# Performance work log

Hardware: AMD Instinct MI355X
Metric: run time of the kernel (lower is better)

## Reference

```python
import jax, jax.numpy as jnp
import numpy as np

B, T, D = 4, 4096, 1024


def setup_inputs() -> dict:
    key = jax.random.key(0)
    ks = jax.random.split(key, 7)
    s_in = 1.0 / np.sqrt(D)
    return {
        "x": jax.random.normal(ks[0], (B, T, D), dtype=jnp.float32),
        "W_in": jax.random.uniform(ks[1], (D, 2 * D), jnp.float32, -s_in, s_in),
        "b_in": jax.random.uniform(ks[2], (2 * D,), jnp.float32, -s_in, s_in),
        "A": jax.random.normal(ks[3], (D,), dtype=jnp.float32),
        "C": jax.random.normal(ks[4], (D,), dtype=jnp.float32),
        "W_out": jax.random.uniform(ks[5], (D, D), jnp.float32, -s_in, s_in),
        "b_out": jax.random.uniform(ks[6], (D,), jnp.float32, -s_in, s_in),
    }


def _ssm(v, A, C):
    # diagonal linear recurrence: h_t = sigmoid(A) * h_{t-1} + v_t ; y_t = C * h_t
    decay = jax.nn.sigmoid(A)  # (D,)
    vT = jnp.swapaxes(v, 0, 1)  # (T, B, D)

    def step(h, vt):
        h = decay * h + vt
        return h, h

    h0 = jnp.zeros(vT.shape[1:], dtype=v.dtype)
    _, hs = jax.lax.scan(step, h0, vT)  # (T, B, D)
    return jnp.swapaxes(hs, 0, 1) * C  # (B, T, D)


def reference(x, W_in, b_in, A, C, W_out, b_out):
    proj = x @ W_in + b_in  # (B, T, 2D)
    v, gate = jnp.split(proj, 2, axis=-1)
    gate = jax.nn.sigmoid(gate)
    y = gate * _ssm(v, A, C)
    return y @ W_out + b_out
```

## Files before the change

kernel.cpp:

```cpp
#include <hip/hip_runtime.h>
#include <math.h>

#define BDIM 4
#define TDIM 4096
#define DDIM 1024
#define MDIM (BDIM * TDIM)

#define NC  64
#define LCH 64
static_assert(NC * LCH == TDIM, "chunking");

typedef __attribute__((ext_vector_type(8))) short short8;
typedef __attribute__((ext_vector_type(4))) float f32x4;

__device__ __forceinline__ unsigned short f2bf(float f) {
  unsigned int u = __float_as_uint(f);
  unsigned int r = (u + 0x7fffu + ((u >> 16) & 1u)) >> 16;
  return (unsigned short)r;
}
__device__ __forceinline__ float bf2f(unsigned short h) {
  return __uint_as_float(((unsigned int)h) << 16);
}
__device__ __forceinline__ float sigmoidf_(float x) {
  return 1.0f / (1.0f + expf(-x));
}

__global__ __launch_bounds__(256) void prep_x_kernel(const float* __restrict__ x,
                                                     unsigned short* __restrict__ xh,
                                                     int n4) {
  int i = blockIdx.x * 256 + threadIdx.x;
  if (i >= n4) return;
  float4 f = ((const float4*)x)[i];
  ushort4 h;
  h.x = f2bf(f.x);
  h.y = f2bf(f.y);
  h.z = f2bf(f.z);
  h.w = f2bf(f.w);
  ((ushort4*)xh)[i] = h;
}

__global__ __launch_bounds__(256) void wprep_kernel(const float* __restrict__ in,
                                                    unsigned short* __restrict__ oh,
                                                    int K, int N) {
  __shared__ float t[64][65];
  int n0 = blockIdx.x * 64;
  int k0 = blockIdx.y * 64;
#pragma unroll
  for (int i = 0; i < 16; ++i) {
    int idx = i * 256 + threadIdx.x;
    int r = idx >> 6, c = idx & 63;
    t[r][c] = in[(size_t)(k0 + r) * N + (n0 + c)];
  }
  __syncthreads();
#pragma unroll
  for (int i = 0; i < 16; ++i) {
    int idx = i * 256 + threadIdx.x;
    int rn = idx >> 6, ck = idx & 63;
    oh[(size_t)(n0 + rn) * K + (k0 + ck)] = f2bf(t[ck][rn]);
  }
}


#define BARRIER()                                  \
  do {                                             \
    asm volatile("" ::: "memory");                 \
    __builtin_amdgcn_s_barrier();                  \
    asm volatile("" ::: "memory");                 \
  } while (0)

#define RD_A(SET, BUFC, H, BK)                                                  \
  _Pragma("unroll") for (int m = 0; m < 4; ++m)                                 \
      SET[m] = *(const short8*)(ldsb + (((BK) ? baseA1 : baseA0) + (BUFC) +     \
                                        (H) * 8192 + m * 2048));

#define RD_B(SET, BUFC, BK)                                                     \
  _Pragma("unroll") for (int n = 0; n < 4; ++n)                                 \
      SET[n] = *(const short8*)(ldsbB + (((BK) ? baseB1 : baseB0) + (BUFC) +    \
                                         n * 2048));

#define MFMA16(ASET, BSET, HH)                                                  \
  __builtin_amdgcn_s_setprio(1);                                                \
  _Pragma("unroll") for (int m = 0; m < 4; ++m)                                 \
      _Pragma("unroll") for (int n = 0; n < 4; ++n)                             \
          acc[(HH) * 4 + m][n] = __builtin_amdgcn_mfma_f32_16x16x32_bf16(       \
              ASET[m], BSET[n], acc[(HH) * 4 + m][n], 0, 0, 0);                 \
  __builtin_amdgcn_s_setprio(0);

#define STAGE(PTR, S, BUFB, KOFF)                                               \
  __builtin_amdgcn_global_load_lds(                                             \
      (const __attribute__((address_space(1))) unsigned int*)((PTR) + off##S +  \
                                                              (KOFF)),         \
      (__attribute__((address_space(3))) unsigned int*)((char*)lds + (BUFB) +   \
                                                        (S) * 8192 +            \
                                                        wave * 1024),           \
      16, 0, 0);

#define TILE(T, BUFC, BUFN)                                                     \
  {                                                                             \
    bool pf = ((T) + 1 < NT);                                                   \
    int k1 = ((T) + 1) << 7;          \
    RD_A(afA, BUFC, 0, 0);                                                      \
    RD_B(bfrA, BUFC, 0);                                                        \
    if (pf) {                                                                   \
      STAGE(AgB, 0, BUFN, k1) STAGE(AgB, 1, BUFN, k1)                           \
      STAGE(AgB, 2, BUFN, k1) STAGE(AgB, 3, BUFN, k1)                           \
    }                                                                           \
    RD_A(afB, BUFC, 1, 0);                                                      \
    MFMA16(afA, bfrA, 0);                                                       \
    if (pf) { STAGE(BgB, 0, 65536 + (BUFN), k1) STAGE(BgB, 1, 65536 + (BUFN), k1) } \
    RD_A(afA, BUFC, 0, 1);                                                      \
    RD_B(bfrB, BUFC, 1);                                                        \
    MFMA16(afB, bfrA, 1);                                                       \
    if (pf) { STAGE(BgB, 2, 65536 + (BUFN), k1) STAGE(BgB, 3, 65536 + (BUFN), k1) } \
    RD_A(afB, BUFC, 1, 1);                                                      \
    MFMA16(afA, bfrB, 0);                                                       \
    MFMA16(afB, bfrB, 1);                                                       \
    if (pf) asm volatile("s_waitcnt vmcnt(0)" ::: "memory");                    \
    BARRIER();                                                                  \
  }

template <int EPI>
__global__ __launch_bounds__(512, 2) void gemm8p(const unsigned short* __restrict__ A,
                                                 const unsigned short* __restrict__ B,
                                                 const float* __restrict__ bias,
                                                 float* __restrict__ outF,
                                                 unsigned short* __restrict__ outV,
                                                 unsigned short* __restrict__ outG,
                                                 int nNt, int K) {
  __shared__ unsigned short lds[65536];

  int cpx = gridDim.x >> 3;
  int bid = blockIdx.x;
  int swz = (bid & 7) * cpx + (bid >> 3);
  int mtile = swz / nNt, ntile = swz % nNt;

  int tid = threadIdx.x;
  int wave = tid >> 6, lane = tid & 63;
  int wm = wave >> 2, wn = wave & 3;
  int rA = wm * 128 + (lane & 15);
  int rB = wn * 64 + (lane & 15);
  int kq2 = (lane >> 4) * 16;

  int baseA0 = ((rA << 7) + kq2) ^ ((rA & 7) << 4);
  int baseA1 = ((rA << 7) + kq2 + 64) ^ ((rA & 7) << 4);
  int baseB0 = ((rB << 7) + kq2) ^ ((rB & 7) << 4);
  int baseB1 = ((rB << 7) + kq2 + 64) ^ ((rB & 7) << 4);
  const char* ldsb = (const char*)lds;
  const char* ldsbB = (const char*)lds + 65536;

#define MKOFF(S) \
  ({ int Lt = (S) * 8192 + tid * 16; int P = Lt ^ (((Lt >> 7) & 7) << 4); \
     ((P >> 7) * (K << 1)) + (P & 127); })
  int off0 = MKOFF(0), off1 = MKOFF(1), off2 = MKOFF(2), off3 = MKOFF(3);
#undef MKOFF

  const char* AgB = (const char*)(A + (size_t)(mtile * 256) * K);
  const char* BgB = (const char*)(B + (size_t)(ntile * 256) * K);

  f32x4 acc[8][4] = {};
  short8 afA[4], afB[4], bfrA[4], bfrB[4];

  STAGE(AgB, 0, 0, 0) STAGE(AgB, 1, 0, 0) STAGE(AgB, 2, 0, 0) STAGE(AgB, 3, 0, 0)
  STAGE(BgB, 0, 65536, 0) STAGE(BgB, 1, 65536, 0)
  STAGE(BgB, 2, 65536, 0) STAGE(BgB, 3, 65536, 0)
  asm volatile("s_waitcnt vmcnt(0)" ::: "memory");
  BARRIER();

  int NT = K >> 6;
  for (int t = 0; t < NT; t += 2) {
    TILE(t, 0, 32768)
    TILE(t + 1, 32768, 0)
  }

  int row0 = mtile * 256 + wm * 128 + ((lane >> 4) << 2);
  int col0 = ntile * 256 + wn * 64 + (lane & 15);
#pragma unroll
  for (int m = 0; m < 8; ++m) {
#pragma unroll
    for (int n = 0; n < 4; ++n) {
      int col = col0 + n * 16;
      float bv = bias[col];
#pragma unroll
      for (int j = 0; j < 4; ++j) {
        int row = row0 + m * 16 + j;
        float val = acc[m][n][j] + bv;
        if (EPI == 0) {
          outF[(size_t)row * (nNt * 256) + col] = val;
        } else {
          if (col < DDIM)
            outV[(size_t)row * DDIM + col] = f2bf(val);
          else
            outG[(size_t)row * DDIM + (col - DDIM)] = f2bf(sigmoidf_(val));
        }
      }
    }
  }
}

__global__ __launch_bounds__(256) void ssm_phase1(const unsigned short* __restrict__ v,
                                                  const float* __restrict__ A,
                                                  float* __restrict__ chunkh) {
  int b = blockIdx.y, c = blockIdx.x;
  int d0 = threadIdx.x * 4;
  float4 a4 = *(const float4*)&A[d0];
  float dx = sigmoidf_(a4.x), dy = sigmoidf_(a4.y), dz = sigmoidf_(a4.z), dw = sigmoidf_(a4.w);
  float hx = 0.f, hy = 0.f, hz = 0.f, hw = 0.f;
  const ushort4* vp = (const ushort4*)(v + ((size_t)b * TDIM + (size_t)c * LCH) * DDIM + d0);
#pragma unroll 4
  for (int i = 0; i < LCH; ++i) {
    ushort4 vv = vp[(size_t)i * (DDIM / 4)];
    hx = fmaf(dx, hx, bf2f(vv.x));
    hy = fmaf(dy, hy, bf2f(vv.y));
    hz = fmaf(dz, hz, bf2f(vv.z));
    hw = fmaf(dw, hw, bf2f(vv.w));
  }
  float4 o = {hx, hy, hz, hw};
  *(float4*)&chunkh[(size_t)(b * NC + c) * DDIM + d0] = o;
}

__global__ __launch_bounds__(256) void ssm_phase2(const float* __restrict__ A,
                                                  float* __restrict__ chunkh) {
  int idx = blockIdx.x * 256 + threadIdx.x;
  int b = idx >> 10, d = idx & 1023;
  float dec = sigmoidf_(A[d]);
  float dL = dec;
#pragma unroll
  for (int i = 0; i < 6; ++i) dL *= dL;
  float hv[NC];
#pragma unroll
  for (int c = 0; c < NC; ++c) hv[c] = chunkh[(size_t)(b * NC + c) * DDIM + d];
  float carry = 0.f;
#pragma unroll
  for (int c = 0; c < NC; ++c) {
    float local = hv[c];
    hv[c] = carry;
    carry = fmaf(dL, carry, local);
  }
#pragma unroll
  for (int c = 0; c < NC; ++c) chunkh[(size_t)(b * NC + c) * DDIM + d] = hv[c];
}

__global__ __launch_bounds__(256) void ssm_phase3(const unsigned short* __restrict__ v,
                                                  const unsigned short* __restrict__ g,
                                                  const float* __restrict__ A,
                                                  const float* __restrict__ C,
                                                  const float* __restrict__ chunkh,
                                                  unsigned short* __restrict__ ybf) {
  int b = blockIdx.y, c = blockIdx.x;
  int d0 = threadIdx.x * 4;
  float4 a4 = *(const float4*)&A[d0];
  float4 c4 = *(const float4*)&C[d0];
  float dx = sigmoidf_(a4.x), dy = sigmoidf_(a4.y), dz = sigmoidf_(a4.z), dw = sigmoidf_(a4.w);
  float4 h0 = *(const float4*)&chunkh[(size_t)(b * NC + c) * DDIM + d0];
  float hx = h0.x, hy = h0.y, hz = h0.z, hw = h0.w;
  size_t base = ((size_t)b * TDIM + (size_t)c * LCH) * DDIM + d0;
  const ushort4* vp = (const ushort4*)(v + base);
  const ushort4* gp = (const ushort4*)(g + base);
  ushort4* yp = (ushort4*)(ybf + base);
#pragma unroll 4
  for (int i = 0; i < LCH; ++i) {
    ushort4 vv = vp[(size_t)i * (DDIM / 4)];
    ushort4 gg = gp[(size_t)i * (DDIM / 4)];
    hx = fmaf(dx, hx, bf2f(vv.x));
    hy = fmaf(dy, hy, bf2f(vv.y));
    hz = fmaf(dz, hz, bf2f(vv.z));
    hw = fmaf(dw, hw, bf2f(vv.w));
    ushort4 yy;
    yy.x = f2bf(bf2f(gg.x) * c4.x * hx);
    yy.y = f2bf(bf2f(gg.y) * c4.y * hy);
    yy.z = f2bf(bf2f(gg.z) * c4.z * hz);
    yy.w = f2bf(bf2f(gg.w) * c4.w * hw);
    yp[(size_t)i * (DDIM / 4)] = yy;
  }
}

extern "C" void kernel_launch(void* const* d_in, const int* in_sizes, int n_in,
                              void* d_out, int out_size, void* d_ws, size_t ws_size,
                              hipStream_t stream) {
  const float* x = (const float*)d_in[0];
  const float* W_in = (const float*)d_in[1];
  const float* b_in = (const float*)d_in[2];
  const float* A = (const float*)d_in[3];
  const float* C = (const float*)d_in[4];
  const float* W_out = (const float*)d_in[5];
  const float* b_out = (const float*)d_in[6];
  float* out = (float*)d_out;

  char* ws = (char*)d_ws;
  const size_t MK = (size_t)MDIM * DDIM;
  unsigned short* xh = (unsigned short*)ws;    ws += MK * 2;
  unsigned short* winh = (unsigned short*)ws;  ws += (size_t)2 * DDIM * DDIM * 2;
  unsigned short* wouth = (unsigned short*)ws; ws += (size_t)DDIM * DDIM * 2;
  unsigned short* v = (unsigned short*)ws;     ws += MK * 2;
  unsigned short* g = (unsigned short*)ws;     ws += MK * 2;
  unsigned short* ybf = (unsigned short*)ws;   ws += MK * 2;
  float* chunkh = (float*)ws;                  ws += (size_t)BDIM * NC * DDIM * 4;

  prep_x_kernel<<<(int)(MK / 4 / 256), 256, 0, stream>>>(x, xh, (int)(MK / 4));
  wprep_kernel<<<dim3(2 * DDIM / 64, DDIM / 64), 256, 0, stream>>>(W_in, winh, DDIM, 2 * DDIM);
  wprep_kernel<<<dim3(DDIM / 64, DDIM / 64), 256, 0, stream>>>(W_out, wouth, DDIM, DDIM);

  gemm8p<1><<<(MDIM / 256) * 8, 512, 0, stream>>>(xh, winh, b_in, nullptr, v, g, 8, DDIM);

  ssm_phase1<<<dim3(NC, BDIM), 256, 0, stream>>>(v, A, chunkh);
  ssm_phase2<<<(BDIM * DDIM) / 256, 256, 0, stream>>>(A, chunkh);
  ssm_phase3<<<dim3(NC, BDIM), 256, 0, stream>>>(v, g, A, C, chunkh, ybf);

  gemm8p<0><<<(MDIM / 256) * 4, 512, 0, stream>>>(ybf, wouth, b_out, out, nullptr, nullptr,
                                                  4, DDIM);
}
```

Baseline: 180.4 us.

## Load B fragments directly from global memory instead of staging through LDS

```diff
diff --git a/kernel.cpp b/kernel.cpp
--- a/kernel.cpp
+++ b/kernel.cpp
@@ -73,11 +73,6 @@
       SET[m] = *(const short8*)(ldsb + (((BK) ? baseA1 : baseA0) + (BUFC) +     \
                                         (H) * 8192 + m * 2048));
 
-#define RD_B(SET, BUFC, BK)                                                     \
-  _Pragma("unroll") for (int n = 0; n < 4; ++n)                                 \
-      SET[n] = *(const short8*)(ldsbB + (((BK) ? baseB1 : baseB0) + (BUFC) +    \
-                                         n * 2048));
-
 #define MFMA16(ASET, BSET, HH)                                                  \
   __builtin_amdgcn_s_setprio(1);                                                \
   _Pragma("unroll") for (int m = 0; m < 4; ++m)                                 \
@@ -86,35 +81,36 @@
               ASET[m], BSET[n], acc[(HH) * 4 + m][n], 0, 0, 0);                 \
   __builtin_amdgcn_s_setprio(0);
 
-#define STAGE(PTR, S, BUFB, KOFF)                                               \
+#define STAGE(S, BUFB, KOFF)                                                    \
   __builtin_amdgcn_global_load_lds(                                             \
-      (const __attribute__((address_space(1))) unsigned int*)((PTR) + off##S +  \
-                                                              (KOFF)),         \
+      (const __attribute__((address_space(1))) unsigned int*)(AgB + off##S +    \
+                                                              (KOFF)),          \
       (__attribute__((address_space(3))) unsigned int*)((char*)lds + (BUFB) +   \
                                                         (S) * 8192 +            \
                                                         wave * 1024),           \
       16, 0, 0);
 
+#define BLOAD(SET, T, KKI)                                                      \
+  _Pragma("unroll") for (int n = 0; n < 4; ++n)                                 \
+      SET[n] = *(const short8*)(B0p + nstride[n] + ((size_t)(T) << 7) +         \
+                                (KKI) * 64);
+
 #define TILE(T, BUFC, BUFN)                                                     \
   {                                                                             \
     bool pf = ((T) + 1 < NT);                                                   \
-    int k1 = ((T) + 1) << 7;          \
+    int k1 = ((T) + 1) << 7;                                                    \
+    BLOAD(b0, T, 0);                                                            \
+    BLOAD(b1, T, 1);                                                            \
+    if (pf) { STAGE(0, BUFN, k1) STAGE(1, BUFN, k1)                             \
+              STAGE(2, BUFN, k1) STAGE(3, BUFN, k1) }                           \
     RD_A(afA, BUFC, 0, 0);                                                      \
-    RD_B(bfrA, BUFC, 0);                                                        \
-    if (pf) {                                                                   \
-      STAGE(AgB, 0, BUFN, k1) STAGE(AgB, 1, BUFN, k1)                           \
-      STAGE(AgB, 2, BUFN, k1) STAGE(AgB, 3, BUFN, k1)                           \
-    }                                                                           \
     RD_A(afB, BUFC, 1, 0);                                                      \
-    MFMA16(afA, bfrA, 0);                                                       \
-    if (pf) { STAGE(BgB, 0, 65536 + (BUFN), k1) STAGE(BgB, 1, 65536 + (BUFN), k1) } \
-    RD_A(afA, BUFC, 0, 1);                                                      \
-    RD_B(bfrB, BUFC, 1);                                                        \
-    MFMA16(afB, bfrA, 1);                                                       \
-    if (pf) { STAGE(BgB, 2, 65536 + (BUFN), k1) STAGE(BgB, 3, 65536 + (BUFN), k1) } \
-    RD_A(afB, BUFC, 1, 1);                                                      \
-    MFMA16(afA, bfrB, 0);                                                       \
-    MFMA16(afB, bfrB, 1);                                                       \
+    MFMA16(afA, b0, 0);                                                         \
+    RD_A(afA2, BUFC, 0, 1);                                                     \
+    MFMA16(afB, b0, 1);                                                         \
+    RD_A(afB2, BUFC, 1, 1);                                                     \
+    MFMA16(afA2, b1, 0);                                                        \
+    MFMA16(afB2, b1, 1);                                                        \
     if (pf) asm volatile("s_waitcnt vmcnt(0)" ::: "memory");                    \
     BARRIER();                                                                  \
   }
@@ -127,7 +123,7 @@
                                                  unsigned short* __restrict__ outV,
                                                  unsigned short* __restrict__ outG,
                                                  int nNt, int K) {
-  __shared__ unsigned short lds[65536];
+  __shared__ unsigned short lds[32768];
 
   int cpx = gridDim.x >> 3;
   int bid = blockIdx.x;
@@ -143,10 +139,7 @@
 
   int baseA0 = ((rA << 7) + kq2) ^ ((rA & 7) << 4);
   int baseA1 = ((rA << 7) + kq2 + 64) ^ ((rA & 7) << 4);
-  int baseB0 = ((rB << 7) + kq2) ^ ((rB & 7) << 4);
-  int baseB1 = ((rB << 7) + kq2 + 64) ^ ((rB & 7) << 4);
   const char* ldsb = (const char*)lds;
-  const char* ldsbB = (const char*)lds + 65536;
 
 #define MKOFF(S) \
   ({ int Lt = (S) * 8192 + tid * 16; int P = Lt ^ (((Lt >> 7) & 7) << 4); \
@@ -155,14 +148,16 @@
 #undef MKOFF
 
   const char* AgB = (const char*)(A + (size_t)(mtile * 256) * K);
-  const char* BgB = (const char*)(B + (size_t)(ntile * 256) * K);
+  const char* B0p =
+      (const char*)B + ((size_t)(ntile * 256 + rB) * K + ((lane >> 4) * 8)) * 2;
+  size_t nstride[4];
+#pragma unroll
+  for (int n = 0; n < 4; ++n) nstride[n] = (size_t)n * ((size_t)K << 5);
 
   f32x4 acc[8][4] = {};
-  short8 afA[4], afB[4], bfrA[4], bfrB[4];
-
-  STAGE(AgB, 0, 0, 0) STAGE(AgB, 1, 0, 0) STAGE(AgB, 2, 0, 0) STAGE(AgB, 3, 0, 0)
-  STAGE(BgB, 0, 65536, 0) STAGE(BgB, 1, 65536, 0)
-  STAGE(BgB, 2, 65536, 0) STAGE(BgB, 3, 65536, 0)
+  short8 afA[4], afB[4], afA2[4], afB2[4], b0[4], b1[4];
+
+  STAGE(0, 0, 0) STAGE(1, 0, 0) STAGE(2, 0, 0) STAGE(3, 0, 0)
   asm volatile("s_waitcnt vmcnt(0)" ::: "memory");
   BARRIER();
 
```

New measurement: 295.4 us. 1.64x slower.

## Restructure GEMM main loop into barrier-synchronized ping-pong schedule with fixed trip count

Applied to the files above, without the earlier changes.

```diff
diff --git a/kernel.cpp b/kernel.cpp
--- a/kernel.cpp
+++ b/kernel.cpp
@@ -95,27 +95,35 @@
                                                         wave * 1024),           \
       16, 0, 0);
 
-#define TILE(T, BUFC, BUFN)                                                     \
+#define TILE8(T, BUFC, BUFN, PF)                                                \
   {                                                                             \
-    bool pf = ((T) + 1 < NT);                                                   \
-    int k1 = ((T) + 1) << 7;          \
+    int k1 = ((T) + 1) << 7;                       \
+                  \
     RD_A(afA, BUFC, 0, 0);                                                      \
-    RD_B(bfrA, BUFC, 0);                                                        \
-    if (pf) {                                                                   \
-      STAGE(AgB, 0, BUFN, k1) STAGE(AgB, 1, BUFN, k1)                           \
-      STAGE(AgB, 2, BUFN, k1) STAGE(AgB, 3, BUFN, k1)                           \
-    }                                                                           \
+    RD_B(bfr, BUFC, 0);                                                         \
+    if (PF) { STAGE(AgB, 0, BUFN, k1) STAGE(AgB, 2, BUFN, k1) }                 \
+    BARRIER();                                                                  \
+    MFMA16(afA, bfr, 0);                                                        \
+    BARRIER();                                                                  \
+                                 \
     RD_A(afB, BUFC, 1, 0);                                                      \
-    MFMA16(afA, bfrA, 0);                                                       \
-    if (pf) { STAGE(BgB, 0, 65536 + (BUFN), k1) STAGE(BgB, 1, 65536 + (BUFN), k1) } \
+    if (PF) { STAGE(AgB, 1, BUFN, k1) STAGE(AgB, 3, BUFN, k1) }                 \
+    BARRIER();                                                                  \
+    MFMA16(afB, bfr, 1);                                                        \
+    BARRIER();                                                                  \
+                          \
     RD_A(afA, BUFC, 0, 1);                                                      \
-    RD_B(bfrB, BUFC, 1);                                                        \
-    MFMA16(afB, bfrA, 1);                                                       \
-    if (pf) { STAGE(BgB, 2, 65536 + (BUFN), k1) STAGE(BgB, 3, 65536 + (BUFN), k1) } \
+    RD_B(bfr, BUFC, 1);                                                         \
+    if (PF) { STAGE(BgB, 0, 65536 + (BUFN), k1) STAGE(BgB, 1, 65536 + (BUFN), k1) \
+              STAGE(BgB, 2, 65536 + (BUFN), k1) STAGE(BgB, 3, 65536 + (BUFN), k1) } \
+    BARRIER();                                                                  \
+    MFMA16(afA, bfr, 0);                                                        \
+    BARRIER();                                                                  \
+                                      \
     RD_A(afB, BUFC, 1, 1);                                                      \
-    MFMA16(afA, bfrB, 0);                                                       \
-    MFMA16(afB, bfrB, 1);                                                       \
-    if (pf) asm volatile("s_waitcnt vmcnt(0)" ::: "memory");                    \
+    BARRIER();                                                                  \
+    MFMA16(afB, bfr, 1);                                                        \
+    if (PF) asm volatile("s_waitcnt vmcnt(0)" ::: "memory");                    \
     BARRIER();                                                                  \
   }
 
@@ -158,7 +166,7 @@
   const char* BgB = (const char*)(B + (size_t)(ntile * 256) * K);
 
   f32x4 acc[8][4] = {};
-  short8 afA[4], afB[4], bfrA[4], bfrB[4];
+  short8 afA[4], afB[4], bfr[4];
 
   STAGE(AgB, 0, 0, 0) STAGE(AgB, 1, 0, 0) STAGE(AgB, 2, 0, 0) STAGE(AgB, 3, 0, 0)
   STAGE(BgB, 0, 65536, 0) STAGE(BgB, 1, 65536, 0)
@@ -166,11 +174,12 @@
   asm volatile("s_waitcnt vmcnt(0)" ::: "memory");
   BARRIER();
 
-  int NT = K >> 6;
-  for (int t = 0; t < NT; t += 2) {
-    TILE(t, 0, 32768)
-    TILE(t + 1, 32768, 0)
-  }
+  for (int t = 0; t < 14; t += 2) {
+    TILE8(t, 0, 32768, 1)
+    TILE8(t + 1, 32768, 0, 1)
+  }
+  TILE8(14, 0, 32768, 1)
+  TILE8(15, 32768, 0, 0)
 
   int row0 = mtile * 256 + wm * 128 + ((lane >> 4) << 2);
   int col0 = ntile * 256 + wn * 64 + (lane & 15);
```

After: 183.9 us. About the same (+1.9%).
